# Performance work log

Hardware: AMD Instinct MI355X
Metric: run time of the kernel (lower is better)

## Reference

```python
import jax, jax.numpy as jnp
import numpy as np

N, C, D = 32768, 2048, 512

def setup_inputs() -> dict:
    key = jax.random.key(0)
    k1, k2, k3 = jax.random.split(key, 3)
    X = jax.random.normal(k1, (N, D), dtype=jnp.float32)
    muK = jax.random.normal(k2, (C, D), dtype=jnp.float32)
    # counts per class; zeros mark 'unvisited' classes exercising the masking path
    cK = jax.random.randint(k3, (C,), 0, 3).astype(jnp.float32)
    return {"X": X, "muK": muK, "cK": cK}

def reference(X, muK, cK):
    # find_dists(A=muK, B=X): dist[i, j] = sum_d (muK[j, d] - X[i, d])**2, scores = -dist
    # avoids materializing the N x C x D broadcast intermediate of the original).
    x2 = jnp.sum(X * X, axis=1, keepdims=True)          # (N, 1)
    m2 = jnp.sum(muK * muK, axis=1)                     # (C,)
    scores = -(x2 + m2[None, :] - 2.0 * (X @ muK.T))    # (N, C)
    # unvisited classes (cK == 0) get per-row min score minus 1
    min_col = jnp.min(scores, axis=1, keepdims=True) - 1.0  # (N, 1)
    scores = jnp.where((cK == 0.0)[None, :], min_col, scores)
    # predict(..., return_probas=True) as used in evaluate_
    return jax.nn.softmax(scores, axis=1)
```

## Files before the change

### kernel.cpp

```cpp
#include <hip/hip_runtime.h>
#include <cfloat>

#define N_ROWS 32768
#define N_CLS  2048
#define DIM    512

typedef __attribute__((ext_vector_type(8))) short short8;
typedef __attribute__((ext_vector_type(4))) short short4v;
typedef __attribute__((ext_vector_type(4))) float f32x4;

__device__ __forceinline__ unsigned f2bf_bits(float x) {
    union { float f; unsigned u; } a; a.f = x;
    return (a.u + 0x7fffu + ((a.u >> 16) & 1u)) >> 16;
}
__device__ __forceinline__ float bf_to_f(unsigned bits) {
    union { unsigned u; float f; } a; a.u = bits << 16;
    return a.f;
}
__device__ __forceinline__ void split_bf(float x, short &h, short &l) {
    unsigned hb = f2bf_bits(x);
    h = (short)hb;
    float r = x - bf_to_f(hb);
    l = (short)f2bf_bits(r);
}

__global__ __launch_bounds__(256) void split_kernel(const float* __restrict__ src,
                                                    short* __restrict__ hi,
                                                    short* __restrict__ lo) {
    int idx = blockIdx.x * 256 + threadIdx.x;
    float4 v = ((const float4*)src)[idx];
    short h0, h1, h2, h3, l0, l1, l2, l3;
    split_bf(v.x, h0, l0); split_bf(v.y, h1, l1);
    split_bf(v.z, h2, l2); split_bf(v.w, h3, l3);
    ((short4v*)hi)[idx] = (short4v){h0, h1, h2, h3};
    ((short4v*)lo)[idx] = (short4v){l0, l1, l2, l3};
}

__global__ __launch_bounds__(256) void m2_kernel(const float* __restrict__ muK,
                                                 float* __restrict__ m2) {
    const int j = blockIdx.x;
    const int t = threadIdx.x;
    const float* r = muK + (size_t)j * DIM;
    float a = r[t], b = r[t + 256];
    float s = a * a + b * b;
    for (int off = 32; off; off >>= 1) s += __shfl_xor(s, off);
    __shared__ float sw[4];
    if ((t & 63) == 0) sw[t >> 6] = s;
    __syncthreads();
    if (t == 0) m2[j] = sw[0] + sw[1] + sw[2] + sw[3];
}

#define GLDS16(g, l) __builtin_amdgcn_global_load_lds( \
    (const __attribute__((address_space(1))) unsigned int*)(g), \
    (__attribute__((address_space(3))) unsigned int*)(l), 16, 0, 0)

__global__ __launch_bounds__(256) void gemm_kernel(const short* __restrict__ Xh,
                                                   const short* __restrict__ Xl,
                                                   const short* __restrict__ Mh,
                                                   const short* __restrict__ Ml,
                                                   const float* __restrict__ m2,
                                                   float* __restrict__ S) {
    __shared__ __align__(16) short As[128 * 32];
    __shared__ __align__(16) short Bs[128 * 32];

    const int tid  = threadIdx.x;
    const int n0   = blockIdx.x * 128;
    const int m0   = blockIdx.y * 128;
    const int w    = tid >> 6;
    const int lane = tid & 63;
    const int wm   = (w >> 1) * 64;
    const int wn   = (w & 1) * 64;
    const int l16  = lane & 15;
    const int quad = lane >> 4;

    const int c0 = w * 128 + lane;
    const int c1 = c0 + 64;
    const size_t ga0 = (size_t)(m0 + (c0 >> 2)) * DIM + (size_t)(((c0 & 3) ^ ((c0 >> 3) & 3)) * 8);
    const size_t ga1 = (size_t)(m0 + (c1 >> 2)) * DIM + (size_t)(((c1 & 3) ^ ((c1 >> 3) & 3)) * 8);
    const size_t gb0 = (size_t)(n0 + (c0 >> 2)) * DIM + (size_t)(((c0 & 3) ^ ((c0 >> 3) & 3)) * 8);
    const size_t gb1 = (size_t)(n0 + (c1 >> 2)) * DIM + (size_t)(((c1 & 3) ^ ((c1 >> 3) & 3)) * 8);

    const int sw = (quad ^ ((l16 >> 1) & 3)) * 8;

    f32x4 acc[4][4];
#pragma unroll
    for (int mt = 0; mt < 4; ++mt)
#pragma unroll
        for (int nt = 0; nt < 4; ++nt)
            acc[mt][nt] = (f32x4){0.f, 0.f, 0.f, 0.f};

#pragma unroll 1
    for (int seg = 0; seg < 3; ++seg) {
        const short* Ap = (seg == 2) ? Xl : Xh;
        const short* Bp = (seg == 1) ? Ml : Mh;
#pragma unroll 1
        for (int kt2 = 0; kt2 < 16; ++kt2) {
            const int kk = kt2 * 32;
            __syncthreads();
            GLDS16(Ap + ga0 + kk, &As[c0 * 8]);
            GLDS16(Ap + ga1 + kk, &As[c1 * 8]);
            GLDS16(Bp + gb0 + kk, &Bs[c0 * 8]);
            GLDS16(Bp + gb1 + kk, &Bs[c1 * 8]);
            __syncthreads();

            short8 ah[4];
#pragma unroll
            for (int mt = 0; mt < 4; ++mt)
                ah[mt] = *(const short8*)&As[(wm + mt * 16 + l16) * 32 + sw];
#pragma unroll
            for (int nt = 0; nt < 4; ++nt) {
                short8 bf = *(const short8*)&Bs[(wn + nt * 16 + l16) * 32 + sw];
#pragma unroll
                for (int mt = 0; mt < 4; ++mt)
                    acc[mt][nt] = __builtin_amdgcn_mfma_f32_16x16x32_bf16(ah[mt], bf, acc[mt][nt], 0, 0, 0);
            }
        }
    }

#pragma unroll
    for (int nt = 0; nt < 4; ++nt) {
        int col = n0 + wn + nt * 16 + l16;
        float mm = m2[col];
#pragma unroll
        for (int mt = 0; mt < 4; ++mt) {
            int rbase = m0 + wm + mt * 16 + quad * 4;
#pragma unroll
            for (int r = 0; r < 4; ++r)
                S[(size_t)(rbase + r) * N_CLS + col] = 2.0f * acc[mt][nt][r] - mm;
        }
    }
}

#define LDR 40
__global__ __launch_bounds__(256) void gemm_fallback(const float* __restrict__ X,
                                                     const float* __restrict__ muK,
                                                     const float* __restrict__ m2,
                                                     float* __restrict__ S) {
    __shared__ __align__(16) short Ah[128 * LDR];
    __shared__ __align__(16) short Al[128 * LDR];
    __shared__ __align__(16) short Bh[128 * LDR];
    __shared__ __align__(16) short Bl[128 * LDR];
    const int tid  = threadIdx.x;
    const int n0   = blockIdx.x * 128;
    const int m0   = blockIdx.y * 128;
    const int w    = tid >> 6;
    const int lane = tid & 63;
    const int wm   = (w >> 1) * 64;
    const int wn   = (w & 1) * 64;
    const int l16  = lane & 15;
    const int quad = lane >> 4;
    f32x4 acc[4][4];
#pragma unroll
    for (int mt = 0; mt < 4; ++mt)
#pragma unroll
        for (int nt = 0; nt < 4; ++nt)
            acc[mt][nt] = (f32x4){0.f, 0.f, 0.f, 0.f};
    for (int kt = 0; kt < DIM; kt += 32) {
        __syncthreads();
#pragma unroll
        for (int i = 0; i < 4; ++i) {
            int idx = tid + 256 * i;
            int row = idx >> 3;
            int c4  = (idx & 7) * 4;
            float4 fa = *(const float4*)(X + (size_t)(m0 + row) * DIM + kt + c4);
            float4 fb = *(const float4*)(muK + (size_t)(n0 + row) * DIM + kt + c4);
            short h0, h1, h2, h3, l0, l1, l2, l3;
            split_bf(fa.x, h0, l0); split_bf(fa.y, h1, l1);
            split_bf(fa.z, h2, l2); split_bf(fa.w, h3, l3);
            *(short4v*)&Ah[row * LDR + c4] = (short4v){h0, h1, h2, h3};
            *(short4v*)&Al[row * LDR + c4] = (short4v){l0, l1, l2, l3};
            split_bf(fb.x, h0, l0); split_bf(fb.y, h1, l1);
            split_bf(fb.z, h2, l2); split_bf(fb.w, h3, l3);
            *(short4v*)&Bh[row * LDR + c4] = (short4v){h0, h1, h2, h3};
            *(short4v*)&Bl[row * LDR + c4] = (short4v){l0, l1, l2, l3};
        }
        __syncthreads();
        short8 ah[4], al[4];
#pragma unroll
        for (int mt = 0; mt < 4; ++mt) {
            int r = wm + mt * 16 + l16;
            ah[mt] = *(const short8*)&Ah[r * LDR + quad * 8];
            al[mt] = *(const short8*)&Al[r * LDR + quad * 8];
        }
#pragma unroll
        for (int nt = 0; nt < 4; ++nt) {
            int r = wn + nt * 16 + l16;
            short8 bh = *(const short8*)&Bh[r * LDR + quad * 8];
            short8 bl = *(const short8*)&Bl[r * LDR + quad * 8];
#pragma unroll
            for (int mt = 0; mt < 4; ++mt)
                acc[mt][nt] = __builtin_amdgcn_mfma_f32_16x16x32_bf16(ah[mt], bh, acc[mt][nt], 0, 0, 0);
#pragma unroll
            for (int mt = 0; mt < 4; ++mt)
                acc[mt][nt] = __builtin_amdgcn_mfma_f32_16x16x32_bf16(ah[mt], bl, acc[mt][nt], 0, 0, 0);
#pragma unroll
            for (int mt = 0; mt < 4; ++mt)
                acc[mt][nt] = __builtin_amdgcn_mfma_f32_16x16x32_bf16(al[mt], bh, acc[mt][nt], 0, 0, 0);
        }
    }
#pragma unroll
    for (int nt = 0; nt < 4; ++nt) {
        int col = n0 + wn + nt * 16 + l16;
        float mm = m2[col];
#pragma unroll
        for (int mt = 0; mt < 4; ++mt) {
            int rbase = m0 + wm + mt * 16 + quad * 4;
#pragma unroll
            for (int r = 0; r < 4; ++r)
                S[(size_t)(rbase + r) * N_CLS + col] = 2.0f * acc[mt][nt][r] - mm;
        }
    }
}

__device__ __forceinline__ void sm_load_row(float* S, int row, int lane, f32x4* v) {
    const f32x4* pi = (const f32x4*)(S + (size_t)row * N_CLS);
#pragma unroll
    for (int i = 0; i < 8; ++i) v[i] = pi[i * 64 + lane];
}

__device__ __forceinline__ void sm_compute_store(float* S, int row, int lane,
                                                 unsigned msk, f32x4* v) {
    float mn = FLT_MAX, mx = -FLT_MAX;
#pragma unroll
    for (int i = 0; i < 8; ++i) {
        f32x4 s = v[i];
        mn = fminf(mn, fminf(fminf(s.x, s.y), fminf(s.z, s.w)));
        if (!((msk >> (i * 4 + 0)) & 1u)) mx = fmaxf(mx, s.x);
        if (!((msk >> (i * 4 + 1)) & 1u)) mx = fmaxf(mx, s.y);
        if (!((msk >> (i * 4 + 2)) & 1u)) mx = fmaxf(mx, s.z);
        if (!((msk >> (i * 4 + 3)) & 1u)) mx = fmaxf(mx, s.w);
    }
    for (int off = 32; off; off >>= 1) {
        mn = fminf(mn, __shfl_xor(mn, off));
        mx = fmaxf(mx, __shfl_xor(mx, off));
    }
    if (mx == -FLT_MAX) mx = mn - 1.0f;
    const float fill = mn - 1.0f;

    float sum = 0.f;
#pragma unroll
    for (int i = 0; i < 8; ++i) {
        f32x4 s = v[i];
        s.x = __expf(((msk >> (i * 4 + 0)) & 1u ? fill : s.x) - mx);
        s.y = __expf(((msk >> (i * 4 + 1)) & 1u ? fill : s.y) - mx);
        s.z = __expf(((msk >> (i * 4 + 2)) & 1u ? fill : s.z) - mx);
        s.w = __expf(((msk >> (i * 4 + 3)) & 1u ? fill : s.w) - mx);
        sum += s.x + s.y + s.z + s.w;
        v[i] = s;
    }
    for (int off = 32; off; off >>= 1) sum += __shfl_xor(sum, off);
    const float inv = 1.0f / sum;
    f32x4* po = (f32x4*)(S + (size_t)row * N_CLS);
#pragma unroll
    for (int i = 0; i < 8; ++i) {
        f32x4 s = v[i] * inv;
        __builtin_nontemporal_store(s, &po[i * 64 + lane]);
    }
}

__global__ __launch_bounds__(256) void softmax_kernel(float* __restrict__ S,
                                                      const float* __restrict__ cK) {
    const int w    = threadIdx.x >> 6;
    const int lane = threadIdx.x & 63;
    const float4* ck4 = (const float4*)cK;

    unsigned msk = 0;
#pragma unroll
    for (int i = 0; i < 8; ++i) {
        float4 k = ck4[i * 64 + lane];
        if (k.x == 0.f) msk |= 1u << (i * 4 + 0);
        if (k.y == 0.f) msk |= 1u << (i * 4 + 1);
        if (k.z == 0.f) msk |= 1u << (i * 4 + 2);
        if (k.w == 0.f) msk |= 1u << (i * 4 + 3);
    }

    const int r0 = blockIdx.x * 16 + w * 4;
    f32x4 va[8], vb[8];

    sm_load_row(S, r0 + 0, lane, va);
    sm_load_row(S, r0 + 1, lane, vb);
    sm_compute_store(S, r0 + 0, lane, msk, va);
    sm_load_row(S, r0 + 2, lane, va);
    sm_compute_store(S, r0 + 1, lane, msk, vb);
    sm_load_row(S, r0 + 3, lane, vb);
    sm_compute_store(S, r0 + 2, lane, msk, va);
    sm_compute_store(S, r0 + 3, lane, msk, vb);
}

extern "C" void kernel_launch(void* const* d_in, const int* in_sizes, int n_in,
                              void* d_out, int out_size, void* d_ws, size_t ws_size,
                              hipStream_t stream) {
    const float* X   = (const float*)d_in[0];
    const float* muK = (const float*)d_in[1];
    const float* cK  = (const float*)d_in[2];
    float* out = (float*)d_out;

    const size_t XN = (size_t)N_ROWS * DIM;
    const size_t MN = (size_t)N_CLS * DIM;
    const size_t need = (2 * XN + 2 * MN) * sizeof(short) + N_CLS * sizeof(float);

    dim3 grid(N_CLS / 128, N_ROWS / 128);

    if (ws_size >= need) {
        short* Xh = (short*)d_ws;
        short* Xl = Xh + XN;
        short* Mh = Xl + XN;
        short* Ml = Mh + MN;
        float* m2 = (float*)(Ml + MN);
        split_kernel<<<(int)(XN / 4 / 256), 256, 0, stream>>>(X, Xh, Xl);
        split_kernel<<<(int)(MN / 4 / 256), 256, 0, stream>>>(muK, Mh, Ml);
        m2_kernel<<<N_CLS, 256, 0, stream>>>(muK, m2);
        gemm_kernel<<<grid, 256, 0, stream>>>(Xh, Xl, Mh, Ml, m2, out);
    } else {
        float* m2f = (float*)d_ws;
        m2_kernel<<<N_CLS, 256, 0, stream>>>(muK, m2f);
        gemm_fallback<<<grid, 256, 0, stream>>>(X, muK, m2f, out);
    }
    softmax_kernel<<<N_ROWS / 16, 256, 0, stream>>>(out, cK);
}
```

Baseline: 626.5 us.

## Fuse three split-bf16 GEMM passes into one K loop with shared tiles

Instead of three sequential passes over K (hi*hi, hi*lo, lo*hi), each staging one A and one B tile, the kernel now loads the hi and lo tiles of both operands per K step and issues all three MFMA groups from them. Each hi tile is reused twice per load, which cuts global/LDS traffic and halves the number of barrier pairs. In exchange LDS use doubles to 32KB per block and register pressure rises from holding both hi and lo fragments, which may lower occupancy.

```diff
diff --git a/kernel.cpp b/kernel.cpp
--- a/kernel.cpp
+++ b/kernel.cpp
@@ -60,8 +60,10 @@
                                                    const short* __restrict__ Ml,
                                                    const float* __restrict__ m2,
                                                    float* __restrict__ S) {
-    __shared__ __align__(16) short As[128 * 32];
-    __shared__ __align__(16) short Bs[128 * 32];
+    __shared__ __align__(16) short Ash[128 * 32];
+    __shared__ __align__(16) short Asl[128 * 32];
+    __shared__ __align__(16) short Bsh[128 * 32];
+    __shared__ __align__(16) short Bsl[128 * 32];
 
     const int tid  = threadIdx.x;
     const int n0   = blockIdx.x * 128;
@@ -90,30 +92,40 @@
             acc[mt][nt] = (f32x4){0.f, 0.f, 0.f, 0.f};
 
 #pragma unroll 1
-    for (int seg = 0; seg < 3; ++seg) {
-        const short* Ap = (seg == 2) ? Xl : Xh;
-        const short* Bp = (seg == 1) ? Ml : Mh;
-#pragma unroll 1
-        for (int kt2 = 0; kt2 < 16; ++kt2) {
-            const int kk = kt2 * 32;
-            __syncthreads();
-            GLDS16(Ap + ga0 + kk, &As[c0 * 8]);
-            GLDS16(Ap + ga1 + kk, &As[c1 * 8]);
-            GLDS16(Bp + gb0 + kk, &Bs[c0 * 8]);
-            GLDS16(Bp + gb1 + kk, &Bs[c1 * 8]);
-            __syncthreads();
-
-            short8 ah[4];
-#pragma unroll
-            for (int mt = 0; mt < 4; ++mt)
-                ah[mt] = *(const short8*)&As[(wm + mt * 16 + l16) * 32 + sw];
-#pragma unroll
-            for (int nt = 0; nt < 4; ++nt) {
-                short8 bf = *(const short8*)&Bs[(wn + nt * 16 + l16) * 32 + sw];
-#pragma unroll
-                for (int mt = 0; mt < 4; ++mt)
-                    acc[mt][nt] = __builtin_amdgcn_mfma_f32_16x16x32_bf16(ah[mt], bf, acc[mt][nt], 0, 0, 0);
-            }
+    for (int kt2 = 0; kt2 < 16; ++kt2) {
+        const int kk = kt2 * 32;
+        __syncthreads();
+        GLDS16(Xh + ga0 + kk, &Ash[c0 * 8]);
+        GLDS16(Xh + ga1 + kk, &Ash[c1 * 8]);
+        GLDS16(Xl + ga0 + kk, &Asl[c0 * 8]);
+        GLDS16(Xl + ga1 + kk, &Asl[c1 * 8]);
+        GLDS16(Mh + gb0 + kk, &Bsh[c0 * 8]);
+        GLDS16(Mh + gb1 + kk, &Bsh[c1 * 8]);
+        GLDS16(Ml + gb0 + kk, &Bsl[c0 * 8]);
+        GLDS16(Ml + gb1 + kk, &Bsl[c1 * 8]);
+        __syncthreads();
+
+        short8 ah[4], al[4];
+#pragma unroll
+        for (int mt = 0; mt < 4; ++mt) {
+            const int ro = (wm + mt * 16 + l16) * 32 + sw;
+            ah[mt] = *(const short8*)&Ash[ro];
+            al[mt] = *(const short8*)&Asl[ro];
+        }
+#pragma unroll
+        for (int nt = 0; nt < 4; ++nt) {
+            const int ro = (wn + nt * 16 + l16) * 32 + sw;
+            short8 bh = *(const short8*)&Bsh[ro];
+            short8 bl = *(const short8*)&Bsl[ro];
+#pragma unroll
+            for (int mt = 0; mt < 4; ++mt)
+                acc[mt][nt] = __builtin_amdgcn_mfma_f32_16x16x32_bf16(ah[mt], bh, acc[mt][nt], 0, 0, 0);
+#pragma unroll
+            for (int mt = 0; mt < 4; ++mt)
+                acc[mt][nt] = __builtin_amdgcn_mfma_f32_16x16x32_bf16(ah[mt], bl, acc[mt][nt], 0, 0, 0);
+#pragma unroll
+            for (int mt = 0; mt < 4; ++mt)
+                acc[mt][nt] = __builtin_amdgcn_mfma_f32_16x16x32_bf16(al[mt], bh, acc[mt][nt], 0, 0, 0);
         }
     }
 
```

After: 586.7 us. 1.07x faster.
